# Kernel tuning notes

Measured on AMD Instinct MI355X. Metric: run time of the kernel, lower is better.

Reference implementation:

```python
import jax, jax.numpy as jnp
import numpy as np

B, N, D_IN, D_HID, D_OUT = 8, 4096, 64, 128, 64
NEG = -1e16


def setup_inputs() -> dict:
    key = jax.random.key(0)
    k1, k2, k3, k4, k5, k6 = jax.random.split(key, 6)
    flow_x = jax.random.normal(k1, (B, N, D_IN), dtype=jnp.float32)
    adj = (jax.random.uniform(k2, (N, N)) < 0.02).astype(jnp.float32)
    graph = adj.at[jnp.arange(N), jnp.arange(N)].set(1.0)
    W1 = jax.random.normal(k3, (D_HID, D_IN), dtype=jnp.float32)
    b1 = jax.random.normal(k4, (D_HID,), dtype=jnp.float32)
    W2 = jax.random.normal(k5, (D_OUT, D_HID), dtype=jnp.float32)
    b2 = jax.random.normal(k6, (D_OUT,), dtype=jnp.float32)
    return {"flow_x": flow_x, "graph": graph, "W1": W1, "b1": b1, "W2": W2, "b2": b2}


def _gat_layer(x, graph, W, b):
    # h = Linear(x) with weight [out,in], no bias
    h = jnp.einsum('bnd,hd->bnh', x, W)
    # dense masked attention scores [B,N,N]
    s = jnp.einsum('bnh,bmh->bnm', h, h) * graph[None]
    s = jnp.where(s == 0.0, NEG, s)  # masked_fill of zeros (torch semantics)
    a = jax.nn.softmax(s, axis=2)
    return jnp.einsum('bnm,bmh->bnh', a, h) + b


def reference(flow_x, graph, W1, b1, W2, b2):
    out = _gat_layer(flow_x, graph, W1, b1)
    out = jax.nn.relu(out)
    out = _gat_layer(out, graph, W2, b2)
    return out[:, :, None, :]  # unsqueeze(2) -> [B, N, 1, D_OUT]
```

## Files before the change

### kernel.cpp

```cpp
#include <hip/hip_runtime.h>
#include <cmath>

#define B_   8
#define N_   4096
#define DIN1 64
#define DHID 128
#define DOUT2 64
#define MAXDEG 256

__device__ __forceinline__ unsigned pack2bf(float a, float b) {
    unsigned ua = __float_as_uint(a), ub = __float_as_uint(b);
    ua = (ua + 0x7FFFu + ((ua >> 16) & 1u)) >> 16;
    ub = (ub + 0x7FFFu + ((ub >> 16) & 1u)) & 0xFFFF0000u;
    return ua | ub;
}
__device__ __forceinline__ float2 unpack2bf(unsigned u) {
    return {__uint_as_float(u << 16), __uint_as_float(u & 0xFFFF0000u)};
}
__device__ __forceinline__ float2 lazy2bf(unsigned u) {
    return {__uint_as_float(u << 16), __uint_as_float(u)};
}

template <int SH>
__device__ __forceinline__ float dpp_shr_add(float p) {
    int t = __builtin_amdgcn_update_dpp(0, __float_as_int(p),
                                        0x110 | SH, 0xF, 0xF, true);
    return p + __int_as_float(t);
}
template <int GRPL>
__device__ __forceinline__ float dpp_reduce(float p) {
    if constexpr (GRPL == 16) p = dpp_shr_add<8>(p);
    p = dpp_shr_add<4>(p);
    p = dpp_shr_add<2>(p);
    p = dpp_shr_add<1>(p);
    return p;
}

__global__ __launch_bounds__(256) void k_build_csr(
    const float* __restrict__ graph, int* __restrict__ cnt, int* __restrict__ idx)
{
    const int wave = threadIdx.x >> 6;
    const int lane = threadIdx.x & 63;
    const int n = blockIdx.x * 4 + wave;
    const unsigned long long below_mask = (1ULL << lane) - 1ULL;

    const float4* __restrict__ row4 = (const float4*)(graph + (size_t)n * N_);
    int* __restrict__ myidx = idx + (size_t)n * MAXDEG;

    int base = 0;
    for (int it = 0; it < N_ / 256; ++it) {
        const int i4 = it * 64 + lane;
        float4 g = row4[i4];
        const int e = 4 * i4;
#pragma unroll
        for (int c = 0; c < 4; ++c) {
            const float gc = (c == 0) ? g.x : (c == 1) ? g.y : (c == 2) ? g.z : g.w;
            const unsigned long long mk = __ballot(gc != 0.0f);
            const int pos = base + __popcll(mk & below_mask);
            if (gc != 0.0f && pos < MAXDEG) myidx[pos] = e + c;
            base += __popcll(mk);
        }
    }
    if (lane == 0) cnt[n] = (base < MAXDEG) ? base : MAXDEG;
}

__global__ __launch_bounds__(256) void k_linear1(
    const float* __restrict__ x, const float* __restrict__ W,
    float* __restrict__ out, void* __restrict__ outb)
{
    constexpr int DIN = DIN1, DOUT = DHID;
    constexpr int CG = DOUT / 4;
    constexpr int RG = 256 / CG;
    constexpr int TR = 32 / RG;

    __shared__ float sWt[DIN][DOUT + 4];

    const int t = threadIdx.x;
    const float4* W4 = (const float4*)W;
    for (int i = t; i < DOUT * (DIN / 4); i += 256) {
        int kk = i / (DIN / 4);
        int d4 = i % (DIN / 4);
        float4 w = W4[i];
        sWt[4 * d4 + 0][kk] = w.x;
        sWt[4 * d4 + 1][kk] = w.y;
        sWt[4 * d4 + 2][kk] = w.z;
        sWt[4 * d4 + 3][kk] = w.w;
    }
    __syncthreads();

    const int rg = t / CG;
    const int c  = t % CG;
    const int base = blockIdx.x * 32;
    const float4* x4 = (const float4*)x;

    float acc[TR][4];
#pragma unroll
    for (int i = 0; i < TR; ++i)
#pragma unroll
        for (int j = 0; j < 4; ++j) acc[i][j] = 0.0f;

    for (int d4 = 0; d4 < DIN / 4; ++d4) {
        float4 xf[TR];
#pragma unroll
        for (int i = 0; i < TR; ++i)
            xf[i] = x4[(size_t)(base + rg * TR + i) * (DIN / 4) + d4];
        float4 wf[4];
#pragma unroll
        for (int dd = 0; dd < 4; ++dd)
            wf[dd] = *(const float4*)&sWt[4 * d4 + dd][4 * c];
#pragma unroll
        for (int i = 0; i < TR; ++i) {
            acc[i][0] += xf[i].x * wf[0].x + xf[i].y * wf[1].x + xf[i].z * wf[2].x + xf[i].w * wf[3].x;
            acc[i][1] += xf[i].x * wf[0].y + xf[i].y * wf[1].y + xf[i].z * wf[2].y + xf[i].w * wf[3].y;
            acc[i][2] += xf[i].x * wf[0].z + xf[i].y * wf[1].z + xf[i].z * wf[2].z + xf[i].w * wf[3].z;
            acc[i][3] += xf[i].x * wf[0].w + xf[i].y * wf[1].w + xf[i].z * wf[2].w + xf[i].w * wf[3].w;
        }
    }

#pragma unroll
    for (int i = 0; i < TR; ++i) {
        const size_t row = (size_t)(base + rg * TR + i);
        float4 o = {acc[i][0], acc[i][1], acc[i][2], acc[i][3]};
        ((float4*)out)[row * CG + c] = o;
        uint2 ob = {pack2bf(o.x, o.y), pack2bf(o.z, o.w)};
        *(uint2*)((char*)outb + row * (DOUT * 2) + c * 8) = ob;
    }
}

template <int DIN, int DOUT>
__global__ __launch_bounds__(256) void k_linear(
    const float* __restrict__ x, const float* __restrict__ W,
    float* __restrict__ out)
{
    constexpr int CG = DOUT / 4;
    constexpr int RG = 256 / CG;
    constexpr int TR = 32 / RG;

    __shared__ float sWt[DIN][DOUT + 4];

    const int t = threadIdx.x;
    const float4* W4 = (const float4*)W;
    for (int i = t; i < DOUT * (DIN / 4); i += 256) {
        int kk = i / (DIN / 4);
        int d4 = i % (DIN / 4);
        float4 w = W4[i];
        sWt[4 * d4 + 0][kk] = w.x;
        sWt[4 * d4 + 1][kk] = w.y;
        sWt[4 * d4 + 2][kk] = w.z;
        sWt[4 * d4 + 3][kk] = w.w;
    }
    __syncthreads();

    const int rg = t / CG;
    const int c  = t % CG;
    const int base = blockIdx.x * 32;
    const float4* x4 = (const float4*)x;

    float acc[TR][4];
#pragma unroll
    for (int i = 0; i < TR; ++i)
#pragma unroll
        for (int j = 0; j < 4; ++j) acc[i][j] = 0.0f;

    for (int d4 = 0; d4 < DIN / 4; ++d4) {
        float4 xf[TR];
#pragma unroll
        for (int i = 0; i < TR; ++i)
            xf[i] = x4[(size_t)(base + rg * TR + i) * (DIN / 4) + d4];
        float4 wf[4];
#pragma unroll
        for (int dd = 0; dd < 4; ++dd)
            wf[dd] = *(const float4*)&sWt[4 * d4 + dd][4 * c];
#pragma unroll
        for (int i = 0; i < TR; ++i) {
            acc[i][0] += xf[i].x * wf[0].x + xf[i].y * wf[1].x + xf[i].z * wf[2].x + xf[i].w * wf[3].x;
            acc[i][1] += xf[i].x * wf[0].y + xf[i].y * wf[1].y + xf[i].z * wf[2].y + xf[i].w * wf[3].y;
            acc[i][2] += xf[i].x * wf[0].z + xf[i].y * wf[1].z + xf[i].z * wf[2].z + xf[i].w * wf[3].z;
            acc[i][3] += xf[i].x * wf[0].w + xf[i].y * wf[1].w + xf[i].z * wf[2].w + xf[i].w * wf[3].w;
        }
    }

#pragma unroll
    for (int i = 0; i < TR; ++i) {
        float4 o = {acc[i][0], acc[i][1], acc[i][2], acc[i][3]};
        ((float4*)out)[(size_t)(base + rg * TR + i) * CG + c] = o;
    }
}

__global__ __launch_bounds__(256) void k_attn1(
    const void* __restrict__ h16, const float* __restrict__ h32,
    const int* __restrict__ cnt, const int* __restrict__ idx,
    const float* __restrict__ bias, float* __restrict__ out)
{
    constexpr int RBb = DHID * 2;
    constexpr int RBf = DHID * 4;
    constexpr int GS  = 4;

    const int bid  = blockIdx.x;
    const int b    = bid & 7;
    const int wave = threadIdx.x >> 6;
    const int lane = threadIdx.x & 63;
    const int n    = (bid >> 3) * 4 + wave;
    const int grp  = lane >> 4;
    const int gl   = lane & 15;
    const int gtop = lane | 15;

    __shared__ int s_off[4][MAXDEG + 48];

    const int k = cnt[n];
    const int* __restrict__ myidx = idx + (size_t)n * MAXDEG;
    for (int j = lane; j < k; j += 64) s_off[wave][j] = myidx[j] * RBb;
    for (int z = k + lane; z < k + 48; z += 64) s_off[wave][z] = 0;

    const char*  __restrict__ hb = (const char*)h16 + (size_t)b * N_ * RBb;
    const char*  __restrict__ hf = (const char*)h32 + (size_t)b * N_ * RBf;
    const int lb = gl * 16;

    float2 qc[4];
    {
        const uint4 qu = *(const uint4*)(hb + (size_t)n * RBb + lb);
        qc[0] = lazy2bf(qu.x); qc[1] = lazy2bf(qu.y);
        qc[2] = lazy2bf(qu.z); qc[3] = lazy2bf(qu.w);
    }

    auto dotc = [&](const float2* c) -> float {
        float2 pa = {0.0f, 0.0f}, pb2 = {0.0f, 0.0f};
        pa.x  += qc[0].x * c[0].x;  pa.y  += qc[0].y * c[0].y;
        pb2.x += qc[1].x * c[1].x;  pb2.y += qc[1].y * c[1].y;
        pa.x  += qc[2].x * c[2].x;  pa.y  += qc[2].y * c[2].y;
        pb2.x += qc[3].x * c[3].x;  pb2.y += qc[3].y * c[3].y;
        return (pa.x + pa.y) + (pb2.x + pb2.y);
    };

    float m;
    {
        float p = dotc(qc);
        p = dpp_reduce<16>(p);
        const float pb = __shfl(p, gtop, 64);
        m = (pb != 0.0f) ? pb : -INFINITY;
    }
    float mt = m - 100.0f;
    float s = 0.0f;
    float acc8[8];
#pragma unroll
    for (int i = 0; i < 8; ++i) acc8[i] = 0.0f;

    auto process = [&](const uint4 cur, int off) {
        float2 c[4] = {lazy2bf(cur.x), lazy2bf(cur.y),
                       lazy2bf(cur.z), lazy2bf(cur.w)};
        float p = dotc(c);
        p = dpp_reduce<16>(p);
        if (__builtin_expect((__ballot(p > mt) & 0x8000800080008000ULL) != 0ULL, 0)) {
            const float pb = __shfl(p, gtop, 64);
            const bool valid = (pb != 0.0f);
            const float pm   = valid ? pb : m;
            const float newm = fmaxf(m, pm);
            const float f = (m == newm) ? 1.0f : __expf(m - newm);
            const float e = valid ? __expf(pb - newm) : 0.0f;
            s = s * f + e;
            const float4* fr = (const float4*)(hf + 2 * (size_t)off) + 2 * gl;
            const float4 lo = fr[0], hi = fr[1];
            const float f8[8] = {lo.x, lo.y, lo.z, lo.w, hi.x, hi.y, hi.z, hi.w};
#pragma unroll
            for (int i = 0; i < 8; ++i) acc8[i] = acc8[i] * f + e * f8[i];
            m = newm;
            mt = m - 100.0f;
        }
    };

    {
        uint4 r0, r1, r2;
        int u0, u1, u2, oA, oB, oC;
        oA = s_off[wave][grp + 2 * GS];
        oB = s_off[wave][grp + 3 * GS];
        u0 = s_off[wave][grp];
        r0 = *(const uint4*)(hb + u0 + lb);
        u1 = s_off[wave][grp + GS];
        r1 = *(const uint4*)(hb + u1 + lb);
        int j = grp;
        while (j < k) {
            oC = s_off[wave][j + 4 * GS];
            u2 = oA; r2 = *(const uint4*)(hb + u2 + lb);
            process(r0, u0);
            j += GS; if (j >= k) break;
            oA = s_off[wave][j + 4 * GS];
            u0 = oB; r0 = *(const uint4*)(hb + u0 + lb);
            process(r1, u1);
            j += GS; if (j >= k) break;
            oB = s_off[wave][j + 4 * GS];
            u1 = oC; r1 = *(const uint4*)(hb + u1 + lb);
            process(r2, u2);
            j += GS;
        }
    }

#pragma unroll
    for (int mask = 16; mask <= 32; mask <<= 1) {
        const float m2 = __shfl_xor(m, mask, 64);
        const float s2 = __shfl_xor(s, mask, 64);
        float a2[8];
#pragma unroll
        for (int i = 0; i < 8; ++i) a2[i] = __shfl_xor(acc8[i], mask, 64);
        const float mm = fmaxf(m, m2);
        const float f1 = (m  == mm) ? 1.0f : __expf(m  - mm);
        const float f2 = (m2 == mm) ? 1.0f : __expf(m2 - mm);
        s = s * f1 + s2 * f2;
#pragma unroll
        for (int i = 0; i < 8; ++i) acc8[i] = acc8[i] * f1 + a2[i] * f2;
        m = mm;
    }

    if (s > 0.0f) {
        if (grp == 0) {
            const float4* bias4 = (const float4*)bias;
            const float4 b0 = bias4[2 * gl], b1 = bias4[2 * gl + 1];
            const float bi[8] = {b0.x, b0.y, b0.z, b0.w, b1.x, b1.y, b1.z, b1.w};
            const float inv = 1.0f / s;
            float4 lo, hi;
            lo.x = fmaxf(acc8[0] * inv + bi[0], 0.0f);
            lo.y = fmaxf(acc8[1] * inv + bi[1], 0.0f);
            lo.z = fmaxf(acc8[2] * inv + bi[2], 0.0f);
            lo.w = fmaxf(acc8[3] * inv + bi[3], 0.0f);
            hi.x = fmaxf(acc8[4] * inv + bi[4], 0.0f);
            hi.y = fmaxf(acc8[5] * inv + bi[5], 0.0f);
            hi.z = fmaxf(acc8[6] * inv + bi[6], 0.0f);
            hi.w = fmaxf(acc8[7] * inv + bi[7], 0.0f);
            float4* orow = (float4*)out + ((size_t)b * N_ + n) * (DHID / 4) + 2 * gl;
            orow[0] = lo;
            orow[1] = hi;
        }
    } else {
        const float4* hf4 = (const float4*)hf;
        const int sl = lane % 32;
        const int rs = lane / 32;
        float4 a = {0.0f, 0.0f, 0.0f, 0.0f};
        for (int row = rs; row < N_; row += 2) {
            float4 v = hf4[(size_t)row * 32 + sl];
            a.x += v.x; a.y += v.y; a.z += v.z; a.w += v.w;
        }
        a.x += __shfl_xor(a.x, 32, 64);
        a.y += __shfl_xor(a.y, 32, 64);
        a.z += __shfl_xor(a.z, 32, 64);
        a.w += __shfl_xor(a.w, 32, 64);
        if (lane < 32) {
            constexpr float invN = 1.0f / (float)N_;
            const float4 bi = ((const float4*)bias)[sl];
            float4 o;
            o.x = fmaxf(a.x * invN + bi.x, 0.0f);
            o.y = fmaxf(a.y * invN + bi.y, 0.0f);
            o.z = fmaxf(a.z * invN + bi.z, 0.0f);
            o.w = fmaxf(a.w * invN + bi.w, 0.0f);
            ((float4*)out)[((size_t)b * N_ + n) * 32 + sl] = o;
        }
    }
}

__global__ __launch_bounds__(256) void k_attn2(
    const float* __restrict__ h, const int* __restrict__ cnt,
    const int* __restrict__ idx, const float* __restrict__ bias,
    float* __restrict__ out)
{
    constexpr int D  = DOUT2;
    constexpr int V  = D / 4;
    constexpr int GS = 4;
    constexpr int RB = D * 4;

    const int bid  = blockIdx.x;
    const int b    = bid & 7;
    const int wave = threadIdx.x >> 6;
    const int lane = threadIdx.x & 63;
    const int n    = (bid >> 3) * 4 + wave;
    const int grp  = lane >> 4;
    const int gl   = lane & 15;
    const int gtop = lane | 15;

    __shared__ int s_off[4][MAXDEG + 48];

    const int k = cnt[n];
    const int* __restrict__ myidx = idx + (size_t)n * MAXDEG;
    for (int j = lane; j < k; j += 64) s_off[wave][j] = myidx[j] * RB;
    for (int z = k + lane; z < k + 48; z += 64) s_off[wave][z] = 0;

    const char* __restrict__ hb = (const char*)h + (size_t)b * N_ * RB;
    const int lb = gl * 16;

    float4 qf;
    qf = *(const float4*)(hb + (size_t)n * RB + lb);

    auto dotc = [&](const float4 c) -> float {
        float pa = qf.x * c.x, pb2 = qf.y * c.y;
        pa += qf.z * c.z;      pb2 += qf.w * c.w;
        return pa + pb2;
    };

    float m;
    {
        float p = dotc(qf);
        p = dpp_reduce<16>(p);
        const float pb = __shfl(p, gtop, 64);
        m = (pb != 0.0f) ? pb : -INFINITY;
    }
    float mt = m - 100.0f;
    float s = 0.0f;
    float4 acc = {0.0f, 0.0f, 0.0f, 0.0f};

    auto process = [&](const float4 cur) {
        float p = dotc(cur);
        p = dpp_reduce<16>(p);
        if (__builtin_expect((__ballot(p > mt) & 0x8000800080008000ULL) != 0ULL, 0)) {
            const float pb = __shfl(p, gtop, 64);
            const bool valid = (pb != 0.0f);
            const float pm   = valid ? pb : m;
            const float newm = fmaxf(m, pm);
            const float f = (m == newm) ? 1.0f : __expf(m - newm);
            const float e = valid ? __expf(pb - newm) : 0.0f;
            s = s * f + e;
            acc.x = acc.x * f + e * cur.x;
            acc.y = acc.y * f + e * cur.y;
            acc.z = acc.z * f + e * cur.z;
            acc.w = acc.w * f + e * cur.w;
            m = newm;
            mt = m - 100.0f;
        }
    };

    {
        float4 r0, r1, r2;
        int oA, oB, oC;
        oA = s_off[wave][grp + 2 * GS];
        oB = s_off[wave][grp + 3 * GS];
        r0 = *(const float4*)(hb + s_off[wave][grp] + lb);
        r1 = *(const float4*)(hb + s_off[wave][grp + GS] + lb);
        int j = grp;
        while (j < k) {
            oC = s_off[wave][j + 4 * GS];
            r2 = *(const float4*)(hb + oA + lb);
            process(r0);
            j += GS; if (j >= k) break;
            oA = s_off[wave][j + 4 * GS];
            r0 = *(const float4*)(hb + oB + lb);
            process(r1);
            j += GS; if (j >= k) break;
            oB = s_off[wave][j + 4 * GS];
            r1 = *(const float4*)(hb + oC + lb);
            process(r2);
            j += GS;
        }
    }

#pragma unroll
    for (int mask = 16; mask <= 32; mask <<= 1) {
        const float m2 = __shfl_xor(m, mask, 64);
        const float s2 = __shfl_xor(s, mask, 64);
        float4 a2;
        a2.x = __shfl_xor(acc.x, mask, 64);
        a2.y = __shfl_xor(acc.y, mask, 64);
        a2.z = __shfl_xor(acc.z, mask, 64);
        a2.w = __shfl_xor(acc.w, mask, 64);
        const float mm = fmaxf(m, m2);
        const float f1 = (m  == mm) ? 1.0f : __expf(m  - mm);
        const float f2 = (m2 == mm) ? 1.0f : __expf(m2 - mm);
        s = s * f1 + s2 * f2;
        acc.x = acc.x * f1 + a2.x * f2;
        acc.y = acc.y * f1 + a2.y * f2;
        acc.z = acc.z * f1 + a2.z * f2;
        acc.w = acc.w * f1 + a2.w * f2;
        m = mm;
    }

    if (s > 0.0f) {
        if (grp == 0) {
            const float4 bi = ((const float4*)bias)[gl];
            const float inv = 1.0f / s;
            float4 o;
            o.x = acc.x * inv + bi.x;
            o.y = acc.y * inv + bi.y;
            o.z = acc.z * inv + bi.z;
            o.w = acc.w * inv + bi.w;
            ((float4*)out)[((size_t)b * N_ + n) * V + gl] = o;
        }
    } else {
        const float4* hb4 = (const float4*)hb;
        const int sl = lane % V;
        const int rs = lane / V;
        float4 a = {0.0f, 0.0f, 0.0f, 0.0f};
        for (int row = rs; row < N_; row += 4) {
            float4 v = hb4[(size_t)row * V + sl];
            a.x += v.x; a.y += v.y; a.z += v.z; a.w += v.w;
        }
#pragma unroll
        for (int mask = 16; mask <= 32; mask <<= 1) {
            a.x += __shfl_xor(a.x, mask, 64);
            a.y += __shfl_xor(a.y, mask, 64);
            a.z += __shfl_xor(a.z, mask, 64);
            a.w += __shfl_xor(a.w, mask, 64);
        }
        if (lane < V) {
            constexpr float invN = 1.0f / (float)N_;
            const float4 bi = ((const float4*)bias)[sl];
            float4 o;
            o.x = a.x * invN + bi.x;
            o.y = a.y * invN + bi.y;
            o.z = a.z * invN + bi.z;
            o.w = a.w * invN + bi.w;
            ((float4*)out)[((size_t)b * N_ + n) * V + sl] = o;
        }
    }
}

extern "C" void kernel_launch(void* const* d_in, const int* in_sizes, int n_in,
                              void* d_out, int out_size, void* d_ws, size_t ws_size,
                              hipStream_t stream) {
    (void)in_sizes; (void)n_in; (void)out_size; (void)ws_size;

    const float* flow_x = (const float*)d_in[0];
    const float* graph  = (const float*)d_in[1];
    const float* W1     = (const float*)d_in[2];
    const float* b1     = (const float*)d_in[3];
    const float* W2     = (const float*)d_in[4];
    const float* b2     = (const float*)d_in[5];
    float* out = (float*)d_out;

    char* p = (char*)d_ws;
    auto carve = [&](size_t bytes) -> void* {
        void* r = (void*)p;
        p += (bytes + 255) & ~(size_t)255;
        return r;
    };
    int*   nbr_cnt = (int*)carve((size_t)N_ * sizeof(int));
    int*   nbr_idx = (int*)carve((size_t)N_ * MAXDEG * sizeof(int));
    float* h1      = (float*)carve((size_t)B_ * N_ * DHID * sizeof(float));
    void*  h1b     = carve((size_t)B_ * N_ * DHID * 2);
    float* x2      = (float*)carve((size_t)B_ * N_ * DHID * sizeof(float));
    float* h2      = (float*)carve((size_t)B_ * N_ * DOUT2 * sizeof(float));

    k_build_csr<<<N_ / 4, 256, 0, stream>>>(graph, nbr_cnt, nbr_idx);

    k_linear1<<<(B_ * N_) / 32, 256, 0, stream>>>(flow_x, W1, h1, h1b);

    k_attn1<<<N_ * B_ / 4, 256, 0, stream>>>(h1b, h1, nbr_cnt, nbr_idx, b1, x2);

    k_linear<DHID, DOUT2><<<(B_ * N_) / 32, 256, 0, stream>>>(x2, W2, h2);

    k_attn2<<<N_ * B_ / 4, 256, 0, stream>>>(h2, nbr_cnt, nbr_idx, b2, out);
}
```

Measured before the change: 224.1 us.

## Process two batches per wave in attn1 and use packed float2 math

Each wave in the first attention kernel now handles the same node for two batches (b and b+4). This reuses the neighbour offset list and its shared-memory staging across both batches and halves the grid. Dot products are written with two-wide vector types so the compiler can emit packed FP32 instructions, in both attention kernels. The cost is roughly double the live registers per thread (two query vectors, two accumulators, two softmax states), which may lower occupancy, and a more branchy update path.

```diff
diff --git a/kernel.cpp b/kernel.cpp
--- a/kernel.cpp
+++ b/kernel.cpp
@@ -8,17 +8,19 @@
 #define DOUT2 64
 #define MAXDEG 256
 
+typedef float f32x2 __attribute__((ext_vector_type(2)));
+
 __device__ __forceinline__ unsigned pack2bf(float a, float b) {
     unsigned ua = __float_as_uint(a), ub = __float_as_uint(b);
     ua = (ua + 0x7FFFu + ((ua >> 16) & 1u)) >> 16;
     ub = (ub + 0x7FFFu + ((ub >> 16) & 1u)) & 0xFFFF0000u;
     return ua | ub;
 }
-__device__ __forceinline__ float2 unpack2bf(unsigned u) {
-    return {__uint_as_float(u << 16), __uint_as_float(u & 0xFFFF0000u)};
-}
-__device__ __forceinline__ float2 lazy2bf(unsigned u) {
-    return {__uint_as_float(u << 16), __uint_as_float(u)};
+__device__ __forceinline__ f32x2 lazy2(unsigned u) {
+    f32x2 r;
+    r.x = __uint_as_float(u << 16);
+    r.y = __uint_as_float(u);
+    return r;
 }
 
 template <int SH>
@@ -195,12 +197,13 @@
     constexpr int RBb = DHID * 2;
     constexpr int RBf = DHID * 4;
     constexpr int GS  = 4;
+    constexpr unsigned long long TM = 0x8000800080008000ULL;
 
     const int bid  = blockIdx.x;
-    const int b    = bid & 7;
+    const int bA   = bid & 3;
     const int wave = threadIdx.x >> 6;
     const int lane = threadIdx.x & 63;
-    const int n    = (bid >> 3) * 4 + wave;
+    const int n    = (bid >> 2) * 4 + wave;
     const int grp  = lane >> 4;
     const int gl   = lane & 15;
     const int gtop = lane | 15;
@@ -212,124 +215,166 @@
     for (int j = lane; j < k; j += 64) s_off[wave][j] = myidx[j] * RBb;
     for (int z = k + lane; z < k + 48; z += 64) s_off[wave][z] = 0;
 
-    const char*  __restrict__ hb = (const char*)h16 + (size_t)b * N_ * RBb;
-    const char*  __restrict__ hf = (const char*)h32 + (size_t)b * N_ * RBf;
+    const char* __restrict__ hbA = (const char*)h16 + (size_t)bA * N_ * RBb;
+    const char* __restrict__ hbB = hbA + (size_t)4 * N_ * RBb;
+    const char* __restrict__ hfA = (const char*)h32 + (size_t)bA * N_ * RBf;
+    const char* __restrict__ hfB = hfA + (size_t)4 * N_ * RBf;
     const int lb = gl * 16;
 
-    float2 qc[4];
+    f32x2 qA[4], qB[4];
     {
-        const uint4 qu = *(const uint4*)(hb + (size_t)n * RBb + lb);
-        qc[0] = lazy2bf(qu.x); qc[1] = lazy2bf(qu.y);
-        qc[2] = lazy2bf(qu.z); qc[3] = lazy2bf(qu.w);
-    }
-
-    auto dotc = [&](const float2* c) -> float {
-        float2 pa = {0.0f, 0.0f}, pb2 = {0.0f, 0.0f};
-        pa.x  += qc[0].x * c[0].x;  pa.y  += qc[0].y * c[0].y;
-        pb2.x += qc[1].x * c[1].x;  pb2.y += qc[1].y * c[1].y;
-        pa.x  += qc[2].x * c[2].x;  pa.y  += qc[2].y * c[2].y;
-        pb2.x += qc[3].x * c[3].x;  pb2.y += qc[3].y * c[3].y;
-        return (pa.x + pa.y) + (pb2.x + pb2.y);
-    };
-
-    float m;
+        const uint4 ua = *(const uint4*)(hbA + (size_t)n * RBb + lb);
+        qA[0] = lazy2(ua.x); qA[1] = lazy2(ua.y);
+        qA[2] = lazy2(ua.z); qA[3] = lazy2(ua.w);
+        const uint4 ub = *(const uint4*)(hbB + (size_t)n * RBb + lb);
+        qB[0] = lazy2(ub.x); qB[1] = lazy2(ub.y);
+        qB[2] = lazy2(ub.z); qB[3] = lazy2(ub.w);
+    }
+
+    auto dot8 = [](const f32x2* q, const f32x2* c) -> float {
+        f32x2 pa = q[0] * c[0];
+        f32x2 pb = q[1] * c[1];
+        pa += q[2] * c[2];
+        pb += q[3] * c[3];
+        f32x2 t = pa + pb;
+        return t.x + t.y;
+    };
+
+    float mA, mB;
     {
-        float p = dotc(qc);
-        p = dpp_reduce<16>(p);
-        const float pb = __shfl(p, gtop, 64);
-        m = (pb != 0.0f) ? pb : -INFINITY;
-    }
-    float mt = m - 100.0f;
-    float s = 0.0f;
-    float acc8[8];
-#pragma unroll
-    for (int i = 0; i < 8; ++i) acc8[i] = 0.0f;
-
-    auto process = [&](const uint4 cur, int off) {
-        float2 c[4] = {lazy2bf(cur.x), lazy2bf(cur.y),
-                       lazy2bf(cur.z), lazy2bf(cur.w)};
-        float p = dotc(c);
-        p = dpp_reduce<16>(p);
-        if (__builtin_expect((__ballot(p > mt) & 0x8000800080008000ULL) != 0ULL, 0)) {
-            const float pb = __shfl(p, gtop, 64);
-            const bool valid = (pb != 0.0f);
-            const float pm   = valid ? pb : m;
-            const float newm = fmaxf(m, pm);
-            const float f = (m == newm) ? 1.0f : __expf(m - newm);
-            const float e = valid ? __expf(pb - newm) : 0.0f;
-            s = s * f + e;
-            const float4* fr = (const float4*)(hf + 2 * (size_t)off) + 2 * gl;
-            const float4 lo = fr[0], hi = fr[1];
-            const float f8[8] = {lo.x, lo.y, lo.z, lo.w, hi.x, hi.y, hi.z, hi.w};
-#pragma unroll
-            for (int i = 0; i < 8; ++i) acc8[i] = acc8[i] * f + e * f8[i];
-            m = newm;
-            mt = m - 100.0f;
+        float pA = dot8(qA, qA);
+        float pB = dot8(qB, qB);
+        pA = dpp_reduce<16>(pA);
+        pB = dpp_reduce<16>(pB);
+        const float ba = __shfl(pA, gtop, 64);
+        const float bb = __shfl(pB, gtop, 64);
+        mA = (ba != 0.0f) ? ba : -INFINITY;
+        mB = (bb != 0.0f) ? bb : -INFINITY;
+    }
+    float mtA = mA - 100.0f, mtB = mB - 100.0f;
+    float sA = 0.0f, sB = 0.0f;
+    float aA[8], aB[8];
+#pragma unroll
+    for (int i = 0; i < 8; ++i) { aA[i] = 0.0f; aB[i] = 0.0f; }
+
+    auto take = [&](float pb, int off, const char* hf,
+                    float& m, float& mt, float& s, float* acc) {
+        const bool valid = (pb != 0.0f);
+        const float pm   = valid ? pb : m;
+        const float newm = fmaxf(m, pm);
+        const float f = (m == newm) ? 1.0f : __expf(m - newm);
+        const float e = valid ? __expf(pb - newm) : 0.0f;
+        s = s * f + e;
+        const float4* fr = (const float4*)(hf + 2 * (size_t)off) + 2 * gl;
+        const float4 lo = fr[0], hi = fr[1];
+        const float f8[8] = {lo.x, lo.y, lo.z, lo.w, hi.x, hi.y, hi.z, hi.w};
+#pragma unroll
+        for (int i = 0; i < 8; ++i) acc[i] = acc[i] * f + e * f8[i];
+        m = newm;
+        mt = m - 100.0f;
+    };
+
+    auto proc2 = [&](const uint4 ca, const uint4 cb, int off) {
+        f32x2 xa[4] = {lazy2(ca.x), lazy2(ca.y), lazy2(ca.z), lazy2(ca.w)};
+        float pA = dot8(qA, xa);
+        f32x2 xb[4] = {lazy2(cb.x), lazy2(cb.y), lazy2(cb.z), lazy2(cb.w)};
+        float pB = dot8(qB, xb);
+        pA = dpp_reduce<16>(pA);
+        pB = dpp_reduce<16>(pB);
+        const unsigned long long tA = __ballot(pA > mtA) & TM;
+        const unsigned long long tB = __ballot(pB > mtB) & TM;
+        if (__builtin_expect((tA | tB) != 0ULL, 0)) {
+            if (tA) take(__shfl(pA, gtop, 64), off, hfA, mA, mtA, sA, aA);
+            if (tB) take(__shfl(pB, gtop, 64), off, hfB, mB, mtB, sB, aB);
         }
     };
 
     {
-        uint4 r0, r1, r2;
-        int u0, u1, u2, oA, oB, oC;
-        oA = s_off[wave][grp + 2 * GS];
-        oB = s_off[wave][grp + 3 * GS];
+        uint4 a0, a1, a2, b0, b1, b2;
+        int u0, u1, u2, f0, f1, f2;
+        f0 = s_off[wave][grp + 2 * GS];
+        f1 = s_off[wave][grp + 3 * GS];
         u0 = s_off[wave][grp];
-        r0 = *(const uint4*)(hb + u0 + lb);
+        a0 = *(const uint4*)(hbA + u0 + lb);
+        b0 = *(const uint4*)(hbB + u0 + lb);
         u1 = s_off[wave][grp + GS];
-        r1 = *(const uint4*)(hb + u1 + lb);
+        a1 = *(const uint4*)(hbA + u1 + lb);
+        b1 = *(const uint4*)(hbB + u1 + lb);
         int j = grp;
         while (j < k) {
-            oC = s_off[wave][j + 4 * GS];
-            u2 = oA; r2 = *(const uint4*)(hb + u2 + lb);
-            process(r0, u0);
+            f2 = s_off[wave][j + 4 * GS];
+            u2 = f0;
+            a2 = *(const uint4*)(hbA + u2 + lb);
+            b2 = *(const uint4*)(hbB + u2 + lb);
+            proc2(a0, b0, u0);
             j += GS; if (j >= k) break;
-            oA = s_off[wave][j + 4 * GS];
-            u0 = oB; r0 = *(const uint4*)(hb + u0 + lb);
-            process(r1, u1);
+            f0 = s_off[wave][j + 4 * GS];
+            u0 = f1;
+            a0 = *(const uint4*)(hbA + u0 + lb);
+            b0 = *(const uint4*)(hbB + u0 + lb);
+            proc2(a1, b1, u1);
             j += GS; if (j >= k) break;
-            oB = s_off[wave][j + 4 * GS];
-            u1 = oC; r1 = *(const uint4*)(hb + u1 + lb);
-            process(r2, u2);
+            f1 = f2;
+            u1 = f2;
+            f1 = s_off[wave][j + 4 * GS];
+            a1 = *(const uint4*)(hbA + u1 + lb);
+            b1 = *(const uint4*)(hbB + u1 + lb);
+            proc2(a2, b2, u2);
             j += GS;
         }
     }
 
 #pragma unroll
     for (int mask = 16; mask <= 32; mask <<= 1) {
-        const float m2 = __shfl_xor(m, mask, 64);
-        const float s2 = __shfl_xor(s, mask, 64);
-        float a2[8];
-#pragma unroll
-        for (int i = 0; i < 8; ++i) a2[i] = __shfl_xor(acc8[i], mask, 64);
-        const float mm = fmaxf(m, m2);
-        const float f1 = (m  == mm) ? 1.0f : __expf(m  - mm);
-        const float f2 = (m2 == mm) ? 1.0f : __expf(m2 - mm);
-        s = s * f1 + s2 * f2;
-#pragma unroll
-        for (int i = 0; i < 8; ++i) acc8[i] = acc8[i] * f1 + a2[i] * f2;
-        m = mm;
-    }
-
-    if (s > 0.0f) {
-        if (grp == 0) {
-            const float4* bias4 = (const float4*)bias;
-            const float4 b0 = bias4[2 * gl], b1 = bias4[2 * gl + 1];
-            const float bi[8] = {b0.x, b0.y, b0.z, b0.w, b1.x, b1.y, b1.z, b1.w};
-            const float inv = 1.0f / s;
-            float4 lo, hi;
-            lo.x = fmaxf(acc8[0] * inv + bi[0], 0.0f);
-            lo.y = fmaxf(acc8[1] * inv + bi[1], 0.0f);
-            lo.z = fmaxf(acc8[2] * inv + bi[2], 0.0f);
-            lo.w = fmaxf(acc8[3] * inv + bi[3], 0.0f);
-            hi.x = fmaxf(acc8[4] * inv + bi[4], 0.0f);
-            hi.y = fmaxf(acc8[5] * inv + bi[5], 0.0f);
-            hi.z = fmaxf(acc8[6] * inv + bi[6], 0.0f);
-            hi.w = fmaxf(acc8[7] * inv + bi[7], 0.0f);
-            float4* orow = (float4*)out + ((size_t)b * N_ + n) * (DHID / 4) + 2 * gl;
-            orow[0] = lo;
-            orow[1] = hi;
-        }
-    } else {
+        const float m2A = __shfl_xor(mA, mask, 64);
+        const float s2A = __shfl_xor(sA, mask, 64);
+        const float m2B = __shfl_xor(mB, mask, 64);
+        const float s2B = __shfl_xor(sB, mask, 64);
+        float xA[8], xB[8];
+#pragma unroll
+        for (int i = 0; i < 8; ++i) {
+            xA[i] = __shfl_xor(aA[i], mask, 64);
+            xB[i] = __shfl_xor(aB[i], mask, 64);
+        }
+        {
+            const float mm = fmaxf(mA, m2A);
+            const float f1 = (mA  == mm) ? 1.0f : __expf(mA  - mm);
+            const float f2 = (m2A == mm) ? 1.0f : __expf(m2A - mm);
+            sA = sA * f1 + s2A * f2;
+#pragma unroll
+            for (int i = 0; i < 8; ++i) aA[i] = aA[i] * f1 + xA[i] * f2;
+            mA = mm;
+        }
+        {
+            const float mm = fmaxf(mB, m2B);
+            const float f1 = (mB  == mm) ? 1.0f : __expf(mB  - mm);
+            const float f2 = (m2B == mm) ? 1.0f : __expf(m2B - mm);
+            sB = sB * f1 + s2B * f2;
+#pragma unroll
+            for (int i = 0; i < 8; ++i) aB[i] = aB[i] * f1 + xB[i] * f2;
+            mB = mm;
+        }
+    }
+
+    auto writerow = [&](int bb, const float* acc, float s) {
+        const float4* bias4 = (const float4*)bias;
+        const float4 b0 = bias4[2 * gl], b1 = bias4[2 * gl + 1];
+        const float bi[8] = {b0.x, b0.y, b0.z, b0.w, b1.x, b1.y, b1.z, b1.w};
+        const float inv = 1.0f / s;
+        float4 lo, hi;
+        lo.x = fmaxf(acc[0] * inv + bi[0], 0.0f);
+        lo.y = fmaxf(acc[1] * inv + bi[1], 0.0f);
+        lo.z = fmaxf(acc[2] * inv + bi[2], 0.0f);
+        lo.w = fmaxf(acc[3] * inv + bi[3], 0.0f);
+        hi.x = fmaxf(acc[4] * inv + bi[4], 0.0f);
+        hi.y = fmaxf(acc[5] * inv + bi[5], 0.0f);
+        hi.z = fmaxf(acc[6] * inv + bi[6], 0.0f);
+        hi.w = fmaxf(acc[7] * inv + bi[7], 0.0f);
+        float4* orow = (float4*)out + ((size_t)bb * N_ + n) * (DHID / 4) + 2 * gl;
+        orow[0] = lo;
+        orow[1] = hi;
+    };
+    auto fallback = [&](int bb, const char* hf) {
         const float4* hf4 = (const float4*)hf;
         const int sl = lane % 32;
         const int rs = lane / 32;
@@ -350,9 +395,14 @@
             o.y = fmaxf(a.y * invN + bi.y, 0.0f);
             o.z = fmaxf(a.z * invN + bi.z, 0.0f);
             o.w = fmaxf(a.w * invN + bi.w, 0.0f);
-            ((float4*)out)[((size_t)b * N_ + n) * 32 + sl] = o;
-        }
-    }
+            ((float4*)out)[((size_t)bb * N_ + n) * 32 + sl] = o;
+        }
+    };
+
+    if (sA > 0.0f) { if (grp == 0) writerow(bA, aA, sA); }
+    if (sB > 0.0f) { if (grp == 1) writerow(bA + 4, aB, sB); }
+    if (sA <= 0.0f) fallback(bA, hfA);
+    if (sB <= 0.0f) fallback(bA + 4, hfB);
 }
 
 __global__ __launch_bounds__(256) void k_attn2(
@@ -386,11 +436,17 @@
 
     float4 qf;
     qf = *(const float4*)(hb + (size_t)n * RB + lb);
+    f32x2 q01, q23;
+    q01.x = qf.x; q01.y = qf.y;
+    q23.x = qf.z; q23.y = qf.w;
 
     auto dotc = [&](const float4 c) -> float {
-        float pa = qf.x * c.x, pb2 = qf.y * c.y;
-        pa += qf.z * c.z;      pb2 += qf.w * c.w;
-        return pa + pb2;
+        f32x2 c01, c23;
+        c01.x = c.x; c01.y = c.y;
+        c23.x = c.z; c23.y = c.w;
+        f32x2 t = q01 * c01;
+        t += q23 * c23;
+        return t.x + t.y;
     };
 
     float m;
@@ -538,7 +594,7 @@
 
     k_linear1<<<(B_ * N_) / 32, 256, 0, stream>>>(flow_x, W1, h1, h1b);
 
-    k_attn1<<<N_ * B_ / 4, 256, 0, stream>>>(h1b, h1, nbr_cnt, nbr_idx, b1, x2);
+    k_attn1<<<N_ * B_ / 8, 256, 0, stream>>>(h1b, h1, nbr_cnt, nbr_idx, b1, x2);
 
     k_linear<DHID, DOUT2><<<(B_ * N_) / 32, 256, 0, stream>>>(x2, W2, h2);
 
```

Measured after the change: 236.1 us. 5.4% more time.

## Prune attention neighbors using a Cauchy-Schwarz norm bound before the gather

Applied to the files above, without the earlier changes.

The linear kernels now also compute and store the L2 norm of each output row. Each attention kernel uses these norms to bound every neighbor's score by |h_n|·|h_j| with a small safety margin. Neighbors whose bound falls below the running max minus 100 would underflow in the softmax, so they are dropped while building the shared-memory neighbor list. This avoids gathering and dot-producting most neighbor rows, at the cost of an extra norm write and read and some reliance on the bound margins being safe for bf16-rounded scores. The dot products are also rewritten with packed two-wide float vectors.

```diff
diff --git a/kernel.cpp b/kernel.cpp
--- a/kernel.cpp
+++ b/kernel.cpp
@@ -8,17 +8,19 @@
 #define DOUT2 64
 #define MAXDEG 256
 
+typedef float f32x2 __attribute__((ext_vector_type(2)));
+
 __device__ __forceinline__ unsigned pack2bf(float a, float b) {
     unsigned ua = __float_as_uint(a), ub = __float_as_uint(b);
     ua = (ua + 0x7FFFu + ((ua >> 16) & 1u)) >> 16;
     ub = (ub + 0x7FFFu + ((ub >> 16) & 1u)) & 0xFFFF0000u;
     return ua | ub;
 }
-__device__ __forceinline__ float2 unpack2bf(unsigned u) {
-    return {__uint_as_float(u << 16), __uint_as_float(u & 0xFFFF0000u)};
-}
-__device__ __forceinline__ float2 lazy2bf(unsigned u) {
-    return {__uint_as_float(u << 16), __uint_as_float(u)};
+__device__ __forceinline__ f32x2 lazy2(unsigned u) {
+    f32x2 r;
+    r.x = __uint_as_float(u << 16);
+    r.y = __uint_as_float(u);
+    return r;
 }
 
 template <int SH>
@@ -66,7 +68,7 @@
 
 __global__ __launch_bounds__(256) void k_linear1(
     const float* __restrict__ x, const float* __restrict__ W,
-    float* __restrict__ out, void* __restrict__ outb)
+    float* __restrict__ out, void* __restrict__ outb, float* __restrict__ nrm)
 {
     constexpr int DIN = DIN1, DOUT = DHID;
     constexpr int CG = DOUT / 4;
@@ -124,13 +126,17 @@
         ((float4*)out)[row * CG + c] = o;
         uint2 ob = {pack2bf(o.x, o.y), pack2bf(o.z, o.w)};
         *(uint2*)((char*)outb + row * (DOUT * 2) + c * 8) = ob;
+        float l2 = o.x * o.x + o.y * o.y + o.z * o.z + o.w * o.w;
+#pragma unroll
+        for (int mk2 = 1; mk2 < CG; mk2 <<= 1) l2 += __shfl_xor(l2, mk2, 64);
+        if (c == 0) nrm[row] = sqrtf(l2);
     }
 }
 
 template <int DIN, int DOUT>
 __global__ __launch_bounds__(256) void k_linear(
     const float* __restrict__ x, const float* __restrict__ W,
-    float* __restrict__ out)
+    float* __restrict__ out, float* __restrict__ nrm)
 {
     constexpr int CG = DOUT / 4;
     constexpr int RG = 256 / CG;
@@ -182,13 +188,19 @@
 
 #pragma unroll
     for (int i = 0; i < TR; ++i) {
+        const size_t row = (size_t)(base + rg * TR + i);
         float4 o = {acc[i][0], acc[i][1], acc[i][2], acc[i][3]};
-        ((float4*)out)[(size_t)(base + rg * TR + i) * CG + c] = o;
+        ((float4*)out)[row * CG + c] = o;
+        float l2 = o.x * o.x + o.y * o.y + o.z * o.z + o.w * o.w;
+#pragma unroll
+        for (int mk2 = 1; mk2 < CG; mk2 <<= 1) l2 += __shfl_xor(l2, mk2, 64);
+        if (c == 0) nrm[row] = sqrtf(l2);
     }
 }
 
 __global__ __launch_bounds__(256) void k_attn1(
     const void* __restrict__ h16, const float* __restrict__ h32,
+    const float* __restrict__ nrm,
     const int* __restrict__ cnt, const int* __restrict__ idx,
     const float* __restrict__ bias, float* __restrict__ out)
 {
@@ -204,51 +216,70 @@
     const int grp  = lane >> 4;
     const int gl   = lane & 15;
     const int gtop = lane | 15;
+    const unsigned long long below = (1ULL << lane) - 1ULL;
 
     __shared__ int s_off[4][MAXDEG + 48];
 
-    const int k = cnt[n];
+    const int kraw = cnt[n];
     const int* __restrict__ myidx = idx + (size_t)n * MAXDEG;
-    for (int j = lane; j < k; j += 64) s_off[wave][j] = myidx[j] * RBb;
-    for (int z = k + lane; z < k + 48; z += 64) s_off[wave][z] = 0;
 
     const char*  __restrict__ hb = (const char*)h16 + (size_t)b * N_ * RBb;
     const char*  __restrict__ hf = (const char*)h32 + (size_t)b * N_ * RBf;
+    const float* __restrict__ nb = nrm + (size_t)b * N_;
     const int lb = gl * 16;
 
-    float2 qc[4];
+    f32x2 qc[4];
     {
         const uint4 qu = *(const uint4*)(hb + (size_t)n * RBb + lb);
-        qc[0] = lazy2bf(qu.x); qc[1] = lazy2bf(qu.y);
-        qc[2] = lazy2bf(qu.z); qc[3] = lazy2bf(qu.w);
-    }
-
-    auto dotc = [&](const float2* c) -> float {
-        float2 pa = {0.0f, 0.0f}, pb2 = {0.0f, 0.0f};
-        pa.x  += qc[0].x * c[0].x;  pa.y  += qc[0].y * c[0].y;
-        pb2.x += qc[1].x * c[1].x;  pb2.y += qc[1].y * c[1].y;
-        pa.x  += qc[2].x * c[2].x;  pa.y  += qc[2].y * c[2].y;
-        pb2.x += qc[3].x * c[3].x;  pb2.y += qc[3].y * c[3].y;
-        return (pa.x + pa.y) + (pb2.x + pb2.y);
+        qc[0] = lazy2(qu.x); qc[1] = lazy2(qu.y);
+        qc[2] = lazy2(qu.z); qc[3] = lazy2(qu.w);
+    }
+
+    auto dot8 = [](const f32x2* q, const f32x2* c) -> float {
+        f32x2 pa = q[0] * c[0];
+        f32x2 pb = q[1] * c[1];
+        pa += q[2] * c[2];
+        pb += q[3] * c[3];
+        f32x2 t = pa + pb;
+        return t.x + t.y;
     };
 
     float m;
     {
-        float p = dotc(qc);
+        float p = dot8(qc, qc);
         p = dpp_reduce<16>(p);
         const float pb = __shfl(p, gtop, 64);
         m = (pb != 0.0f) ? pb : -INFINITY;
     }
     float mt = m - 100.0f;
+
+    int kk = 0;
+    {
+        const bool keepall = (m == -INFINITY);
+        const float sq = keepall ? 0.0f : sqrtf(m) * 1.001f;
+        for (int j0 = 0; j0 < kraw; j0 += 64) {
+            const int j = j0 + lane;
+            bool keep = false;
+            int id = 0;
+            if (j < kraw) {
+                id = myidx[j];
+                keep = keepall || (nb[id] * sq * 1.02f + 4.0f > mt);
+            }
+            const unsigned long long mk = __ballot(keep);
+            if (keep) s_off[wave][kk + __popcll(mk & below)] = id * RBb;
+            kk += __popcll(mk);
+        }
+        for (int z = kk + lane; z < kk + 48; z += 64) s_off[wave][z] = 0;
+    }
+
     float s = 0.0f;
     float acc8[8];
 #pragma unroll
     for (int i = 0; i < 8; ++i) acc8[i] = 0.0f;
 
     auto process = [&](const uint4 cur, int off) {
-        float2 c[4] = {lazy2bf(cur.x), lazy2bf(cur.y),
-                       lazy2bf(cur.z), lazy2bf(cur.w)};
-        float p = dotc(c);
+        f32x2 c[4] = {lazy2(cur.x), lazy2(cur.y), lazy2(cur.z), lazy2(cur.w)};
+        float p = dot8(qc, c);
         p = dpp_reduce<16>(p);
         if (__builtin_expect((__ballot(p > mt) & 0x8000800080008000ULL) != 0ULL, 0)) {
             const float pb = __shfl(p, gtop, 64);
@@ -278,15 +309,15 @@
         u1 = s_off[wave][grp + GS];
         r1 = *(const uint4*)(hb + u1 + lb);
         int j = grp;
-        while (j < k) {
+        while (j < kk) {
             oC = s_off[wave][j + 4 * GS];
             u2 = oA; r2 = *(const uint4*)(hb + u2 + lb);
             process(r0, u0);
-            j += GS; if (j >= k) break;
+            j += GS; if (j >= kk) break;
             oA = s_off[wave][j + 4 * GS];
             u0 = oB; r0 = *(const uint4*)(hb + u0 + lb);
             process(r1, u1);
-            j += GS; if (j >= k) break;
+            j += GS; if (j >= kk) break;
             oB = s_off[wave][j + 4 * GS];
             u1 = oC; r1 = *(const uint4*)(hb + u1 + lb);
             process(r2, u2);
@@ -356,9 +387,9 @@
 }
 
 __global__ __launch_bounds__(256) void k_attn2(
-    const float* __restrict__ h, const int* __restrict__ cnt,
-    const int* __restrict__ idx, const float* __restrict__ bias,
-    float* __restrict__ out)
+    const float* __restrict__ h, const float* __restrict__ nrm,
+    const int* __restrict__ cnt, const int* __restrict__ idx,
+    const float* __restrict__ bias, float* __restrict__ out)
 {
     constexpr int D  = DOUT2;
     constexpr int V  = D / 4;
@@ -373,24 +404,30 @@
     const int grp  = lane >> 4;
     const int gl   = lane & 15;
     const int gtop = lane | 15;
+    const unsigned long long below = (1ULL << lane) - 1ULL;
 
     __shared__ int s_off[4][MAXDEG + 48];
 
-    const int k = cnt[n];
+    const int kraw = cnt[n];
     const int* __restrict__ myidx = idx + (size_t)n * MAXDEG;
-    for (int j = lane; j < k; j += 64) s_off[wave][j] = myidx[j] * RB;
-    for (int z = k + lane; z < k + 48; z += 64) s_off[wave][z] = 0;
-
-    const char* __restrict__ hb = (const char*)h + (size_t)b * N_ * RB;
+
+    const char*  __restrict__ hb = (const char*)h + (size_t)b * N_ * RB;
+    const float* __restrict__ nb = nrm + (size_t)b * N_;
     const int lb = gl * 16;
 
     float4 qf;
     qf = *(const float4*)(hb + (size_t)n * RB + lb);
+    f32x2 q01, q23;
+    q01.x = qf.x; q01.y = qf.y;
+    q23.x = qf.z; q23.y = qf.w;
 
     auto dotc = [&](const float4 c) -> float {
-        float pa = qf.x * c.x, pb2 = qf.y * c.y;
-        pa += qf.z * c.z;      pb2 += qf.w * c.w;
-        return pa + pb2;
+        f32x2 c01, c23;
+        c01.x = c.x; c01.y = c.y;
+        c23.x = c.z; c23.y = c.w;
+        f32x2 t = q01 * c01;
+        t += q23 * c23;
+        return t.x + t.y;
     };
 
     float m;
@@ -401,6 +438,26 @@
         m = (pb != 0.0f) ? pb : -INFINITY;
     }
     float mt = m - 100.0f;
+
+    int kk = 0;
+    {
+        const bool keepall = (m == -INFINITY);
+        const float sq = keepall ? 0.0f : sqrtf(m) * 1.001f;
+        for (int j0 = 0; j0 < kraw; j0 += 64) {
+            const int j = j0 + lane;
+            bool keep = false;
+            int id = 0;
+            if (j < kraw) {
+                id = myidx[j];
+                keep = keepall || (nb[id] * sq * 1.01f + 4.0f > mt);
+            }
+            const unsigned long long mk = __ballot(keep);
+            if (keep) s_off[wave][kk + __popcll(mk & below)] = id * RB;
+            kk += __popcll(mk);
+        }
+        for (int z = kk + lane; z < kk + 48; z += 64) s_off[wave][z] = 0;
+    }
+
     float s = 0.0f;
     float4 acc = {0.0f, 0.0f, 0.0f, 0.0f};
 
@@ -432,15 +489,15 @@
         r0 = *(const float4*)(hb + s_off[wave][grp] + lb);
         r1 = *(const float4*)(hb + s_off[wave][grp + GS] + lb);
         int j = grp;
-        while (j < k) {
+        while (j < kk) {
             oC = s_off[wave][j + 4 * GS];
             r2 = *(const float4*)(hb + oA + lb);
             process(r0);
-            j += GS; if (j >= k) break;
+            j += GS; if (j >= kk) break;
             oA = s_off[wave][j + 4 * GS];
             r0 = *(const float4*)(hb + oB + lb);
             process(r1);
-            j += GS; if (j >= k) break;
+            j += GS; if (j >= kk) break;
             oB = s_off[wave][j + 4 * GS];
             r1 = *(const float4*)(hb + oC + lb);
             process(r2);
@@ -533,14 +590,16 @@
     void*  h1b     = carve((size_t)B_ * N_ * DHID * 2);
     float* x2      = (float*)carve((size_t)B_ * N_ * DHID * sizeof(float));
     float* h2      = (float*)carve((size_t)B_ * N_ * DOUT2 * sizeof(float));
+    float* nrm1    = (float*)carve((size_t)B_ * N_ * sizeof(float));
+    float* nrm2    = (float*)carve((size_t)B_ * N_ * sizeof(float));
 
     k_build_csr<<<N_ / 4, 256, 0, stream>>>(graph, nbr_cnt, nbr_idx);
 
-    k_linear1<<<(B_ * N_) / 32, 256, 0, stream>>>(flow_x, W1, h1, h1b);
-
-    k_attn1<<<N_ * B_ / 4, 256, 0, stream>>>(h1b, h1, nbr_cnt, nbr_idx, b1, x2);
-
-    k_linear<DHID, DOUT2><<<(B_ * N_) / 32, 256, 0, stream>>>(x2, W2, h2);
-
-    k_attn2<<<N_ * B_ / 4, 256, 0, stream>>>(h2, nbr_cnt, nbr_idx, b2, out);
-}
+    k_linear1<<<(B_ * N_) / 32, 256, 0, stream>>>(flow_x, W1, h1, h1b, nrm1);
+
+    k_attn1<<<N_ * B_ / 4, 256, 0, stream>>>(h1b, h1, nrm1, nbr_cnt, nbr_idx, b1, x2);
+
+    k_linear<DHID, DOUT2><<<(B_ * N_) / 32, 256, 0, stream>>>(x2, W2, h2, nrm2);
+
+    k_attn2<<<N_ * B_ / 4, 256, 0, stream>>>(h2, nrm2, nbr_cnt, nbr_idx, b2, out);
+}
```

Measured after the change: 247.9 us. 10.6% more time.
